# Kernel tuning notes

Measured on AMD Instinct MI355X. Metric: run time of the kernel, lower is better.

The kernel has to match this reference:

```python
import jax, jax.numpy as jnp
import numpy as np

D_MODEL = 256
D_STATE = 64
D_CONV = 4
EXPAND = 2
HEADDIM = 64
D_INNER = EXPAND * D_MODEL            # 512
NHEADS = D_INNER // HEADDIM           # 8
D_XBC = D_INNER + 2 * D_STATE         # 640 (x, B, C; ngroups=1)
D_IN_PROJ = 2 * D_INNER + 2 * D_STATE + NHEADS  # 1160


def setup_inputs() -> dict:
    key = jax.random.key(0)
    ks = jax.random.split(key, 8)
    x = jax.random.normal(ks[0], (64, 5000, 12), jnp.float32)
    W_in = jax.random.normal(ks[1], (D_MODEL, D_IN_PROJ), jnp.float32) * 0.02
    conv_w = jax.random.normal(ks[2], (D_XBC, D_CONV), jnp.float32) * 0.1
    conv_b = jnp.zeros((D_XBC,), jnp.float32)
    A_log = jnp.log(jax.random.uniform(ks[3], (NHEADS,), jnp.float32, 1.0, 16.0))
    dt_bias = jax.random.normal(ks[4], (NHEADS,), jnp.float32) * 0.1
    D = jnp.ones((NHEADS,), jnp.float32)
    norm_w = jnp.ones((D_INNER,), jnp.float32)
    W_out = jax.random.normal(ks[5], (D_INNER, D_MODEL), jnp.float32) * 0.02
    return {"x": x, "W_in": W_in, "conv_w": conv_w, "conv_b": conv_b,
            "A_log": A_log, "dt_bias": dt_bias, "D": D,
            "norm_w": norm_w, "W_out": W_out}


def _mamba2(u, W_in, conv_w, conv_b, A_log, dt_bias, D, norm_w, W_out):
    b, l, _ = u.shape
    zxbcdt = u @ W_in                                   # (b,l,1160)
    z = zxbcdt[..., :D_INNER]                           # (b,l,512)
    xBC = zxbcdt[..., D_INNER:D_INNER + D_XBC]          # (b,l,640)
    dt = zxbcdt[..., D_INNER + D_XBC:]                  # (b,l,8)
    # causal depthwise conv1d (kernel 4) + SiLU
    xp = jnp.pad(xBC, ((0, 0), (D_CONV - 1, 0), (0, 0)))
    xBC = sum(xp[:, k:k + l, :] * conv_w[:, k] for k in range(D_CONV)) + conv_b
    xBC = jax.nn.silu(xBC)
    xs = xBC[..., :D_INNER].reshape(b, l, NHEADS, HEADDIM)
    Bm = xBC[..., D_INNER:D_INNER + D_STATE]            # (b,l,64)
    Cm = xBC[..., D_INNER + D_STATE:]                   # (b,l,64)
    dt = jax.nn.softplus(dt + dt_bias)                  # (b,l,h)
    A = -jnp.exp(A_log)                                 # (h,)

    def step(h, inp):
        x_t, dt_t, B_t, C_t = inp                       # (b,h,p),(b,h),(b,n),(b,n)
        decay = jnp.exp(dt_t * A)                       # (b,h)
        h = h * decay[..., None, None] + (dt_t[..., None] * x_t)[..., None] * B_t[:, None, None, :]
        y = jnp.einsum('bhpn,bn->bhp', h, C_t)
        return h, y

    h0 = jnp.zeros((b, NHEADS, HEADDIM, D_STATE), u.dtype)
    _, ys = jax.lax.scan(step, h0, (xs.transpose(1, 0, 2, 3), dt.transpose(1, 0, 2),
                                    Bm.transpose(1, 0, 2), Cm.transpose(1, 0, 2)))
    y = ys.transpose(1, 0, 2, 3) + D[None, None, :, None] * xs   # D skip, per head
    y = y.reshape(b, l, D_INNER)
    # RMSNormGated: gate then rmsnorm
    y = y * jax.nn.silu(z)
    y = y * jax.lax.rsqrt(jnp.mean(y * y, axis=-1, keepdims=True) + 1e-5) * norm_w
    return y @ W_out                                    # (b,l,256)


def reference(x, W_in, conv_w, conv_b, A_log, dt_bias, D, norm_w, W_out):
    b = x.shape[0]
    u = x.reshape(b, 250, 240)                          # 'b (t p1) f -> b t (p1 f)'
    u = jnp.pad(u, ((0, 0), (0, 0), (0, D_MODEL - 240)))
    y = _mamba2(u, W_in, conv_w, conv_b, A_log, dt_bias, D, norm_w, W_out)
    y = jax.nn.selu(y)                                  # AlphaDropout is identity at eval
    y = y[..., :240]
    return y.reshape(b, 5000, 12)
```

## Files before the change

### kernel.cpp

```cpp
#include <hip/hip_runtime.h>
#include <cstdint>
#include <cstddef>

#define D_MODEL 256
#define D_STATE 64
#define HEADDIM 64
#define D_INNER 512
#define NHEADS 8
#define D_XBC 640
#define NPROJ 1160
#define ZXW 1152
#define BATCH 64
#define SEQ 250
#define ROWS (BATCH * SEQ)
#define KIN 240
#define KPAD 256
#define NPAD 1216
#define TPAD 256

typedef __bf16 bf16x8 __attribute__((ext_vector_type(8)));
typedef float f32x4 __attribute__((ext_vector_type(4)));

__device__ __forceinline__ float readlane_f(float v, int lane) {
    return __uint_as_float(__builtin_amdgcn_readlane(__float_as_uint(v), lane));
}
__device__ __forceinline__ float silu_f(float x) { return x * (1.f / (1.f + __expf(-x))); }
__device__ __forceinline__ unsigned short bf16_rne(float f) {
    unsigned int u = __float_as_uint(f);
    u += 0x7fff + ((u >> 16) & 1);
    return (unsigned short)(u >> 16);
}
__device__ __forceinline__ float bf2f(unsigned short u) {
    return __uint_as_float(((unsigned int)u) << 16);
}
__device__ __forceinline__ unsigned int pack2(float a, float b) {
    return (unsigned int)bf16_rne(a) | ((unsigned int)bf16_rne(b) << 16);
}

__global__ __launch_bounds__(256) void cast_w_kernel(const float* __restrict__ Win,
                                                     unsigned short* __restrict__ bt_bf) {
    int idx = blockIdx.x * 256 + threadIdx.x;
    int n = idx >> 8, k = idx & 255;
    float v = (n < NPROJ && k < KIN) ? Win[k * NPROJ + n] : 0.f;
    bt_bf[idx] = bf16_rne(v);
}

#define SB 272
__global__ __launch_bounds__(256) void gemm1_mfma(const float* __restrict__ X,
                                                  const unsigned short* __restrict__ Bt,
                                                  unsigned short* __restrict__ Czx,
                                                  float* __restrict__ dtraw) {
    __shared__ unsigned short S[64 * SB];
    const int tid = threadIdx.x;
    const int lane = tid & 63, w = tid >> 6;
    const int q = lane >> 4, l15 = lane & 15;
    const int rowBase = blockIdx.x * 64;

    {
        const int r = tid >> 2, seg = tid & 3;
        const float* xr = X + (size_t)(rowBase + r) * KIN;
#pragma unroll
        for (int i = 0; i < 15; i++) {
            int c4 = seg * 15 + i;
            float4 v = *(const float4*)&xr[c4 * 4];
            unsigned short t4[4];
            t4[0] = bf16_rne(v.x); t4[1] = bf16_rne(v.y);
            t4[2] = bf16_rne(v.z); t4[3] = bf16_rne(v.w);
            *(uint2*)&S[r * SB + c4 * 4] = *(uint2*)t4;
        }
        if (seg < 2) {
            uint4 z = {0, 0, 0, 0};
            *(uint4*)&S[r * SB + 240 + seg * 8] = z;
        }
    }
    __syncthreads();
    bf16x8 afr[8];
#pragma unroll
    for (int kk = 0; kk < 8; kk++)
        afr[kk] = *(const bf16x8*)&S[(w * 16 + l15) * SB + kk * 32 + q * 8];
    __syncthreads();

    for (int j = 0; j < 19; j++) {
        {
            const int r = tid >> 2, seg = tid & 3;
            const unsigned short* br = Bt + (size_t)(j * 64 + r) * KPAD;
#pragma unroll
            for (int i = 0; i < 8; i++) {
                int c = seg * 8 + i * 32;
                int cs = (c ^ ((r & 3) << 3));
                *(uint4*)&S[r * SB + cs] = *(const uint4*)&br[c];
            }
        }
        __syncthreads();
        f32x4 acc[4] = {};
#pragma unroll
        for (int kk = 0; kk < 8; kk++) {
#pragma unroll
            for (int nt = 0; nt < 4; nt++) {
                int row = nt * 16 + l15;
                int c = kk * 32 + q * 8;
                int cs = (c ^ ((row & 3) << 3));
                bf16x8 bfr = *(const bf16x8*)&S[row * SB + cs];
                acc[nt] = __builtin_amdgcn_mfma_f32_16x16x32_bf16(afr[kk], bfr,
                                                                  acc[nt], 0, 0, 0);
            }
        }
        __syncthreads();

        if (j < 18) {
#pragma unroll
            for (int nt = 0; nt < 4; nt++) {
                int gcol = j * 64 + nt * 16 + l15;
#pragma unroll
                for (int reg = 0; reg < 4; reg++) {
                    int grow = rowBase + w * 16 + q * 4 + reg;
                    unsigned int u = bf16_rne(acc[nt][reg]);
                    unsigned int partner = (unsigned int)__shfl_xor((int)u, 1, 64);
                    if ((l15 & 1) == 0)
                        *(unsigned int*)&Czx[(size_t)grow * ZXW + gcol] =
                            u | (partner << 16);
                }
            }
        } else {
            if (l15 < 8) {
#pragma unroll
                for (int reg = 0; reg < 4; reg++) {
                    int grow = rowBase + w * 16 + q * 4 + reg;
                    dtraw[(size_t)grow * NHEADS + l15] = acc[0][reg];
                }
            }
        }
    }
}

#define CT_IN_STR 68
#define CT_TR_STR 70
__global__ __launch_bounds__(256) void conv_kernel(const unsigned short* __restrict__ zxbc,
                                                   const float* __restrict__ dtraw,
                                                   const float* __restrict__ conv_w,
                                                   const float* __restrict__ conv_b,
                                                   const float* __restrict__ dt_bias,
                                                   unsigned short* __restrict__ xc_bf,
                                                   unsigned short* __restrict__ xcT_bf,
                                                   float* __restrict__ dtp) {
    const int b = blockIdx.x;
    const int t0 = blockIdx.z * 64;
    if (blockIdx.y == 10) {
        for (int it = threadIdx.x; it < 512; it += 256) {
            int h = it & 7;
            int t = t0 + (it >> 3);
            if (t < SEQ) {
                float v = dtraw[(size_t)(b * SEQ + t) * NHEADS + h] + dt_bias[h];
                dtp[(size_t)(b * SEQ + t) * NHEADS + h] =
                    (v > 20.f) ? v : __logf(1.f + __expf(v));
            }
        }
        return;
    }
    __shared__ float In[67 * CT_IN_STR];
    __shared__ unsigned short OutT[64 * CT_TR_STR];
    const int cg = blockIdx.y;
    const int tid = threadIdx.x;
    const int lane = tid & 63;
    const int w = tid >> 6;
    const int ch = cg * 64 + lane;

    for (int r = w; r < 67; r += 4) {
        int t = t0 - 3 + r;
        float v = (t >= 0 && t < SEQ)
                      ? bf2f(zxbc[(size_t)(b * SEQ + t) * ZXW + D_INNER + ch])
                      : 0.f;
        In[r * CT_IN_STR + lane] = v;
    }
    __syncthreads();
    const float w0 = conv_w[ch * 4 + 0], w1 = conv_w[ch * 4 + 1];
    const float w2 = conv_w[ch * 4 + 2], w3 = conv_w[ch * 4 + 3];
    const float bias = conv_b[ch];
    unsigned short vals[16];
#pragma unroll
    for (int i = 0; i < 16; i++) {
        int tt = w * 16 + i;
        float acc = fmaf(w3, In[(tt + 3) * CT_IN_STR + lane],
                    fmaf(w2, In[(tt + 2) * CT_IN_STR + lane],
                    fmaf(w1, In[(tt + 1) * CT_IN_STR + lane],
                    fmaf(w0, In[tt * CT_IN_STR + lane], bias))));
        float sv = silu_f(acc);
        unsigned short bv = (t0 + tt < SEQ) ? bf16_rne(sv) : (unsigned short)0;
        vals[i] = bv;
        OutT[lane * CT_TR_STR + tt] = bv;
    }
#pragma unroll
    for (int i = 0; i < 16; i++) {
        int tt = w * 16 + i;
        if (t0 + tt < SEQ)
            xc_bf[(size_t)(b * SEQ + t0 + tt) * D_XBC + ch] = vals[i];
    }
    __syncthreads();
    unsigned short* dstbase = xcT_bf + ((size_t)b * D_XBC + cg * 64) * TPAD + t0;
#pragma unroll
    for (int i = 0; i < 16; i++) {
        int c2 = w * 16 + i;
        dstbase[(size_t)c2 * TPAD + lane] = OutT[c2 * CT_TR_STR + lane];
    }
}

#define LSTR 72
__global__ __launch_bounds__(256) void scan_intra(const unsigned short* __restrict__ xc_bf,
                                                  const unsigned short* __restrict__ xcT_bf,
                                                  const float* __restrict__ dtp,
                                                  const float* __restrict__ A_log,
                                                  const float* __restrict__ Dvec,
                                                  unsigned short* __restrict__ yout_bf,
                                                  unsigned short* __restrict__ st_g) {
    __shared__ unsigned short C_l[64 * LSTR];
    __shared__ unsigned short BP_l[64 * LSTR];
    __shared__ unsigned short XT_l[64 * LSTR];
    __shared__ float cs_s[64], dts_s[64], fws_s[64];

    const int blk = blockIdx.x;
    const int bh = blk >> 2, c = blk & 3;
    const int b = bh >> 3, h = bh & 7;
    const int tid = threadIdx.x;
    const int lane = tid & 63, w = tid >> 6;
    const int q = lane >> 4, l15 = lane & 15;
    const int t0 = c * 64;
    const float A = -__expf(A_log[h]);
    const float Dh = Dvec[h];

    const int r = tid >> 2, c0 = (tid & 3) * 16;

    {
        if (t0 + r < SEQ) {
            const unsigned short* rowp = xc_bf + (size_t)(b * SEQ + t0 + r) * D_XBC;
            *(uint4*)&C_l[r * LSTR + c0] = *(const uint4*)&rowp[D_INNER + D_STATE + c0];
            *(uint4*)&C_l[r * LSTR + c0 + 8] =
                *(const uint4*)&rowp[D_INNER + D_STATE + c0 + 8];
            *(uint4*)&BP_l[r * LSTR + c0] = *(const uint4*)&rowp[D_INNER + c0];
            *(uint4*)&BP_l[r * LSTR + c0 + 8] = *(const uint4*)&rowp[D_INNER + c0 + 8];
        } else {
            uint4 z = {0, 0, 0, 0};
            *(uint4*)&C_l[r * LSTR + c0] = z;
            *(uint4*)&C_l[r * LSTR + c0 + 8] = z;
            *(uint4*)&BP_l[r * LSTR + c0] = z;
            *(uint4*)&BP_l[r * LSTR + c0 + 8] = z;
        }
        const unsigned short* xrow =
            xcT_bf + ((size_t)b * D_XBC + h * HEADDIM + r) * TPAD + t0;
        *(uint4*)&XT_l[r * LSTR + c0] = *(const uint4*)&xrow[c0];
        *(uint4*)&XT_l[r * LSTR + c0 + 8] = *(const uint4*)&xrow[c0 + 8];
    }
    uint4 braw0, braw1;
    {
        const unsigned short* brow =
            xcT_bf + ((size_t)b * D_XBC + D_INNER + r) * TPAD + t0 + c0;
        braw0 = *(const uint4*)&brow[0];
        braw1 = *(const uint4*)&brow[8];
    }
    if (w == 0) {
        int t = lane;
        float dtv = (t0 + t < SEQ) ? dtp[(size_t)(b * SEQ + t0 + t) * NHEADS + h] : 0.f;
        float csv = dtv * A;
#pragma unroll
        for (int o = 1; o < 64; o <<= 1) {
            float u = __shfl_up(csv, o, 64);
            if (lane >= o) csv += u;
        }
        float tot = readlane_f(csv, 63);
        cs_s[t] = csv;
        dts_s[t] = dtv;
        fws_s[t] = dtv * __expf(tot - csv);
    }
    __syncthreads();

    f32x4 g[4] = {};
#pragma unroll
    for (int k0 = 0; k0 < 64; k0 += 32) {
        bf16x8 ca = *(const bf16x8*)&C_l[(w * 16 + l15) * LSTR + k0 + q * 8];
#pragma unroll
        for (int nt = 0; nt < 4; nt++) {
            bf16x8 bb = *(const bf16x8*)&BP_l[(nt * 16 + l15) * LSTR + k0 + q * 8];
            g[nt] = __builtin_amdgcn_mfma_f32_16x16x32_bf16(ca, bb, g[nt], 0, 0, 0);
        }
    }
    __syncthreads();

    {
        unsigned short tmp[16];
        const unsigned short* rp = (const unsigned short*)&braw0;
#pragma unroll
        for (int j = 0; j < 8; j++) tmp[j] = bf16_rne(bf2f(rp[j]) * fws_s[c0 + j]);
        rp = (const unsigned short*)&braw1;
#pragma unroll
        for (int j = 0; j < 8; j++) tmp[8 + j] = bf16_rne(bf2f(rp[j]) * fws_s[c0 + 8 + j]);
        *(uint4*)&C_l[r * LSTR + c0] = *(uint4*)&tmp[0];
        *(uint4*)&C_l[r * LSTR + c0 + 8] = *(uint4*)&tmp[8];
    }
#pragma unroll
    for (int nt = 0; nt < 4; nt++) {
#pragma unroll
        for (int rr = 0; rr < 4; rr++) {
            int t = w * 16 + q * 4 + rr;
            int s = nt * 16 + l15;
            float pv = 0.f;
            if (s <= t) {
                pv = g[nt][rr] * __expf(cs_s[t] - cs_s[s]) * dts_s[s];
                if (s == t) pv += Dh;
            }
            unsigned int u = bf16_rne(pv);
            unsigned int partner = (unsigned int)__shfl_xor((int)u, 1, 64);
            if ((l15 & 1) == 0)
                *(unsigned int*)&BP_l[t * LSTR + nt * 16 + l15] = u | (partner << 16);
        }
    }
    __syncthreads();

    f32x4 y[4] = {};
#pragma unroll
    for (int k0 = 0; k0 < 64; k0 += 32) {
        bf16x8 pa = *(const bf16x8*)&BP_l[(w * 16 + l15) * LSTR + k0 + q * 8];
#pragma unroll
        for (int nt = 0; nt < 4; nt++) {
            bf16x8 xb = *(const bf16x8*)&XT_l[(nt * 16 + l15) * LSTR + k0 + q * 8];
            y[nt] = __builtin_amdgcn_mfma_f32_16x16x32_bf16(pa, xb, y[nt], 0, 0, 0);
        }
    }
    if (c < 3) {
        f32x4 st[4] = {};
#pragma unroll
        for (int k0 = 0; k0 < 64; k0 += 32) {
            bf16x8 xa = *(const bf16x8*)&XT_l[(w * 16 + l15) * LSTR + k0 + q * 8];
#pragma unroll
            for (int nt = 0; nt < 4; nt++) {
                bf16x8 bwb = *(const bf16x8*)&C_l[(nt * 16 + l15) * LSTR + k0 + q * 8];
                st[nt] = __builtin_amdgcn_mfma_f32_16x16x32_bf16(xa, bwb, st[nt], 0, 0, 0);
            }
        }
        unsigned short* stc = st_g + ((size_t)(bh * 3 + c)) * 4096;
#pragma unroll
        for (int nt = 0; nt < 4; nt++)
#pragma unroll
            for (int rr = 0; rr < 4; rr++) {
                unsigned int u = bf16_rne(st[nt][rr]);
                unsigned int partner = (unsigned int)__shfl_xor((int)u, 1, 64);
                if ((l15 & 1) == 0)
                    *(unsigned int*)&stc[(w * 16 + q * 4 + rr) * 64 + nt * 16 + l15] =
                        u | (partner << 16);
            }
    }
#pragma unroll
    for (int nt = 0; nt < 4; nt++)
#pragma unroll
        for (int rr = 0; rr < 4; rr++) {
            int t = w * 16 + q * 4 + rr;
            if (t0 + t < SEQ) {
                int p = nt * 16 + l15;
                unsigned int u = bf16_rne(y[nt][rr]);
                unsigned int partner = (unsigned int)__shfl_xor((int)u, 1, 64);
                if ((l15 & 1) == 0)
                    *(unsigned int*)&yout_bf[(size_t)(b * SEQ + t0 + t) * D_INNER +
                                             h * HEADDIM + p] = u | (partner << 16);
            }
        }
}

__global__ __launch_bounds__(256) void scan_inter(const unsigned short* __restrict__ xc_bf,
                                                  const float* __restrict__ dtp,
                                                  const float* __restrict__ A_log,
                                                  unsigned short* __restrict__ yout_bf,
                                                  const unsigned short* __restrict__ st_g) {
    __shared__ unsigned short C_l[64 * LSTR];
    __shared__ unsigned short h_l[64 * LSTR];
    __shared__ float cs_s[64];
    __shared__ float csum[4];

    const int blk = blockIdx.x;
    const int bh = blk / 3, c = (blk - bh * 3) + 1;
    const int b = bh >> 3, h = bh & 7;
    const int tid = threadIdx.x;
    const int lane = tid & 63, w = tid >> 6;
    const int q = lane >> 4, l15 = lane & 15;
    const int t0 = c * 64;
    const float A = -__expf(A_log[h]);

    {
        int t = lane;
        int gt = w * 64 + t;
        float dtv = (gt < SEQ) ? dtp[(size_t)(b * SEQ + gt) * NHEADS + h] : 0.f;
        float csv = dtv * A;
#pragma unroll
        for (int o = 1; o < 64; o <<= 1) {
            float u = __shfl_up(csv, o, 64);
            if (lane >= o) csv += u;
        }
        if (w == c) cs_s[t] = csv;
        if (lane == 63) csum[w] = csv;
    }
    {
        int r = tid >> 2, c0 = (tid & 3) * 16;
        if (t0 + r < SEQ) {
            const unsigned short* rowp = xc_bf + (size_t)(b * SEQ + t0 + r) * D_XBC;
            *(uint4*)&C_l[r * LSTR + c0] = *(const uint4*)&rowp[D_INNER + D_STATE + c0];
            *(uint4*)&C_l[r * LSTR + c0 + 8] =
                *(const uint4*)&rowp[D_INNER + D_STATE + c0 + 8];
        } else {
            uint4 z = {0, 0, 0, 0};
            *(uint4*)&C_l[r * LSTR + c0] = z;
            *(uint4*)&C_l[r * LSTR + c0 + 8] = z;
        }
    }
    __syncthreads();

    {
        float wgt[3];
        for (int cp = 0; cp < c; cp++) {
            float s = 0.f;
            for (int j = cp + 1; j < c; j++) s += csum[j];
            wgt[cp] = __expf(s);
        }
        const unsigned short* stb = st_g + (size_t)bh * 3 * 4096;
        for (int i = tid; i < 4096; i += 256) {
            float acc = 0.f;
            for (int cp = 0; cp < c; cp++) acc += wgt[cp] * bf2f(stb[cp * 4096 + i]);
            h_l[(i >> 6) * LSTR + (i & 63)] = bf16_rne(acc);
        }
    }
    __syncthreads();

    f32x4 in[4] = {};
#pragma unroll
    for (int k0 = 0; k0 < 64; k0 += 32) {
        bf16x8 ca = *(const bf16x8*)&C_l[(w * 16 + l15) * LSTR + k0 + q * 8];
#pragma unroll
        for (int nt = 0; nt < 4; nt++) {
            bf16x8 hb = *(const bf16x8*)&h_l[(nt * 16 + l15) * LSTR + k0 + q * 8];
            in[nt] = __builtin_amdgcn_mfma_f32_16x16x32_bf16(ca, hb, in[nt], 0, 0, 0);
        }
    }
#pragma unroll
    for (int nt = 0; nt < 4; nt++)
#pragma unroll
        for (int r = 0; r < 4; r++) {
            int t = w * 16 + q * 4 + r;
            if (t0 + t < SEQ) {
                int p = nt * 16 + l15;
                size_t ai = (size_t)(b * SEQ + t0 + t) * D_INNER + h * HEADDIM + p;
                float alpha = __expf(cs_s[t]);
                float nv = bf2f(yout_bf[ai]) + alpha * in[nt][r];
                unsigned int u = bf16_rne(nv);
                unsigned int partner = (unsigned int)__shfl_xor((int)u, 1, 64);
                if ((l15 & 1) == 0)
                    *(unsigned int*)&yout_bf[ai] = u | (partner << 16);
            }
        }
}

__global__ __launch_bounds__(256) void wcast_kernel(const float* __restrict__ Wout,
                                                    unsigned short* __restrict__ wt_bf) {
    int idx = blockIdx.x * 256 + threadIdx.x;
    int n = idx & 255, k = idx >> 8;
    wt_bf[n * D_INNER + k] = bf16_rne(Wout[k * D_MODEL + n]);
}

__global__ __launch_bounds__(256) void gate_kernel(const unsigned short* __restrict__ yout_bf,
                                                   const unsigned short* __restrict__ zxbc,
                                                   const float* __restrict__ norm_w,
                                                   unsigned short* __restrict__ g_bf) {
    const int wid = threadIdx.x >> 6, lane = threadIdx.x & 63;
    const int row = blockIdx.x * 4 + wid;
    const unsigned short* yr = yout_bf + (size_t)row * D_INNER;
    const unsigned short* zr = zxbc + (size_t)row * ZXW;
    const int c0 = lane * 8;
    uint4 yp = *(const uint4*)&yr[c0];
    uint4 zp = *(const uint4*)&zr[c0];
    const unsigned short* ys = (const unsigned short*)&yp;
    const unsigned short* zs = (const unsigned short*)&zp;
    float g[8];
#pragma unroll
    for (int i = 0; i < 8; i++) g[i] = bf2f(ys[i]) * silu_f(bf2f(zs[i]));
    float s = 0.f;
#pragma unroll
    for (int i = 0; i < 8; i++) s = fmaf(g[i], g[i], s);
#pragma unroll
    for (int o = 32; o; o >>= 1) s += __shfl_xor(s, o, 64);
    float rms = rsqrtf(s * (1.f / 512.f) + 1e-5f);
    float4 w0 = *(const float4*)&norm_w[c0], w1 = *(const float4*)&norm_w[c0 + 4];
    uint4 pk;
    pk.x = pack2(g[0] * rms * w0.x, g[1] * rms * w0.y);
    pk.y = pack2(g[2] * rms * w0.z, g[3] * rms * w0.w);
    pk.z = pack2(g[4] * rms * w1.x, g[5] * rms * w1.y);
    pk.w = pack2(g[6] * rms * w1.z, g[7] * rms * w1.w);
    *(uint4*)&g_bf[(size_t)row * D_INNER + c0] = pk;
}

#define SA 40
__global__ __launch_bounds__(256) void gemm2_mfma(const unsigned short* __restrict__ A,
                                                  const unsigned short* __restrict__ Bt,
                                                  float* __restrict__ out) {
    __shared__ unsigned short As[128 * SA];
    __shared__ unsigned short Bs[64 * SA];
    const int tid = threadIdx.x;
    const int lane = tid & 63, wave = tid >> 6;
    const int wm = wave >> 1, wn = wave & 1;
    const int q = lane >> 4, l15 = lane & 15;
    const int rowBase = blockIdx.y * 128, colBase = blockIdx.x * 64;
    f32x4 acc[4][2] = {};

    const int sr = tid >> 2;
    const int sc = (tid & 3) * 8;

    for (int k0 = 0; k0 < D_INNER; k0 += 32) {
        *(float4*)&As[sr * SA + sc] =
            *(const float4*)&A[(size_t)(rowBase + sr) * D_INNER + k0 + sc];
        *(float4*)&As[(sr + 64) * SA + sc] =
            *(const float4*)&A[(size_t)(rowBase + sr + 64) * D_INNER + k0 + sc];
        *(float4*)&Bs[sr * SA + sc] =
            *(const float4*)&Bt[(size_t)(colBase + sr) * D_INNER + k0 + sc];
        __syncthreads();

        bf16x8 bfr[2];
#pragma unroll
        for (int nt = 0; nt < 2; nt++)
            bfr[nt] = *(const bf16x8*)&Bs[(wn * 32 + nt * 16 + l15) * SA + q * 8];
#pragma unroll
        for (int mt = 0; mt < 4; mt++) {
            bf16x8 afr = *(const bf16x8*)&As[(wm * 64 + mt * 16 + l15) * SA + q * 8];
#pragma unroll
            for (int nt = 0; nt < 2; nt++)
                acc[mt][nt] = __builtin_amdgcn_mfma_f32_16x16x32_bf16(afr, bfr[nt],
                                                                      acc[mt][nt], 0, 0, 0);
        }
        __syncthreads();
    }
    const float SC = 1.0507009873554805f, AL = 1.6732632423543772f;
#pragma unroll
    for (int mt = 0; mt < 4; mt++) {
        int grow = rowBase + wm * 64 + mt * 16 + q * 4;
#pragma unroll
        for (int nt = 0; nt < 2; nt++) {
            int gcol = colBase + wn * 32 + nt * 16 + l15;
            if (gcol < 240) {
#pragma unroll
                for (int reg = 0; reg < 4; reg++) {
                    float v = acc[mt][nt][reg];
                    v = (v > 0.f) ? SC * v : SC * AL * (__expf(v) - 1.f);
                    out[(size_t)(grow + reg) * 240 + gcol] = v;
                }
            }
        }
    }
}

extern "C" void kernel_launch(void* const* d_in, const int* in_sizes, int n_in,
                              void* d_out, int out_size, void* d_ws, size_t ws_size,
                              hipStream_t stream) {
    const float* x = (const float*)d_in[0];
    const float* W_in = (const float*)d_in[1];
    const float* conv_w = (const float*)d_in[2];
    const float* conv_b = (const float*)d_in[3];
    const float* A_log = (const float*)d_in[4];
    const float* dt_bias = (const float*)d_in[5];
    const float* Dv = (const float*)d_in[6];
    const float* norm_w = (const float*)d_in[7];
    const float* W_out = (const float*)d_in[8];
    float* out = (float*)d_out;

    unsigned short* us = (unsigned short*)d_ws;
    unsigned short* zxbc_bf = us;
    unsigned short* xc_bf = zxbc_bf + (size_t)ROWS * ZXW;
    unsigned short* xcT_bf = xc_bf + (size_t)ROWS * D_XBC;
    unsigned short* yout_bf = xcT_bf + (size_t)BATCH * D_XBC * TPAD;
    unsigned short* st_g = yout_bf + (size_t)ROWS * D_INNER;
    unsigned short* bt_bf = st_g + (size_t)512 * 3 * 4096;
    unsigned short* wt_bf = bt_bf + (size_t)NPAD * KPAD;
    unsigned short* g_bf = wt_bf + (size_t)D_MODEL * D_INNER;
    float* dtraw = (float*)(g_bf + (size_t)ROWS * D_INNER);
    float* dtp = dtraw + (size_t)ROWS * NHEADS;

    cast_w_kernel<<<dim3(NPAD * KPAD / 256), 256, 0, stream>>>(W_in, bt_bf);

    gemm1_mfma<<<dim3(ROWS / 64), 256, 0, stream>>>(x, bt_bf, zxbc_bf, dtraw);

    conv_kernel<<<dim3(BATCH, 11, 4), 256, 0, stream>>>(zxbc_bf, dtraw, conv_w, conv_b,
                                                        dt_bias, xc_bf, xcT_bf, dtp);

    scan_intra<<<dim3(BATCH * NHEADS * 4), 256, 0, stream>>>(xc_bf, xcT_bf, dtp, A_log, Dv,
                                                             yout_bf, st_g);

    scan_inter<<<dim3(BATCH * NHEADS * 3), 256, 0, stream>>>(xc_bf, dtp, A_log,
                                                             yout_bf, st_g);

    wcast_kernel<<<dim3(D_INNER * D_MODEL / 256), 256, 0, stream>>>(W_out, wt_bf);

    gate_kernel<<<dim3(ROWS / 4), 256, 0, stream>>>(yout_bf, zxbc_bf, norm_w, g_bf);

    gemm2_mfma<<<dim3(D_MODEL / 64, ROWS / 128), 256, 0, stream>>>(g_bf, wt_bf, out);
}
```

Measured before the change: 223.2 us.

## Split gemm1 column tiles across two blocks, prefetch B into registers, transpose MFMA output

```diff
diff --git a/kernel.cpp b/kernel.cpp
--- a/kernel.cpp
+++ b/kernel.cpp
@@ -54,10 +54,13 @@
     const int tid = threadIdx.x;
     const int lane = tid & 63, w = tid >> 6;
     const int q = lane >> 4, l15 = lane & 15;
-    const int rowBase = blockIdx.x * 64;
-
-    {
-        const int r = tid >> 2, seg = tid & 3;
+    const int rowBase = blockIdx.y * 64;
+    const int jBeg = blockIdx.x * 10;
+    const int jEnd = (jBeg + 10 < 19) ? jBeg + 10 : 19;
+
+    const int r = tid >> 2, seg = tid & 3;
+
+    {
         const float* xr = X + (size_t)(rowBase + r) * KIN;
 #pragma unroll
         for (int i = 0; i < 15; i++) {
@@ -78,20 +81,31 @@
 #pragma unroll
     for (int kk = 0; kk < 8; kk++)
         afr[kk] = *(const bf16x8*)&S[(w * 16 + l15) * SB + kk * 32 + q * 8];
-    __syncthreads();
-
-    for (int j = 0; j < 19; j++) {
-        {
-            const int r = tid >> 2, seg = tid & 3;
-            const unsigned short* br = Bt + (size_t)(j * 64 + r) * KPAD;
-#pragma unroll
-            for (int i = 0; i < 8; i++) {
-                int c = seg * 8 + i * 32;
-                int cs = (c ^ ((r & 3) << 3));
-                *(uint4*)&S[r * SB + cs] = *(const uint4*)&br[c];
-            }
-        }
+
+    uint4 breg[8];
+    {
+        const unsigned short* br = Bt + (size_t)(jBeg * 64 + r) * KPAD;
+#pragma unroll
+        for (int i = 0; i < 8; i++)
+            breg[i] = *(const uint4*)&br[seg * 8 + i * 32];
+    }
+
+    for (int j = jBeg; j < jEnd; j++) {
         __syncthreads();
+#pragma unroll
+        for (int i = 0; i < 8; i++) {
+            int c = seg * 8 + i * 32;
+            int cs = c ^ ((r & 3) << 3);
+            *(uint4*)&S[r * SB + cs] = breg[i];
+        }
+        if (j + 1 < jEnd) {
+            const unsigned short* br = Bt + (size_t)((j + 1) * 64 + r) * KPAD;
+#pragma unroll
+            for (int i = 0; i < 8; i++)
+                breg[i] = *(const uint4*)&br[seg * 8 + i * 32];
+        }
+        __syncthreads();
+
         f32x4 acc[4] = {};
 #pragma unroll
         for (int kk = 0; kk < 8; kk++) {
@@ -99,36 +113,26 @@
             for (int nt = 0; nt < 4; nt++) {
                 int row = nt * 16 + l15;
                 int c = kk * 32 + q * 8;
-                int cs = (c ^ ((row & 3) << 3));
+                int cs = c ^ ((row & 3) << 3);
                 bf16x8 bfr = *(const bf16x8*)&S[row * SB + cs];
-                acc[nt] = __builtin_amdgcn_mfma_f32_16x16x32_bf16(afr[kk], bfr,
+                acc[nt] = __builtin_amdgcn_mfma_f32_16x16x32_bf16(bfr, afr[kk],
                                                                   acc[nt], 0, 0, 0);
             }
         }
-        __syncthreads();
-
+        const int grow = rowBase + w * 16 + l15;
         if (j < 18) {
 #pragma unroll
             for (int nt = 0; nt < 4; nt++) {
-                int gcol = j * 64 + nt * 16 + l15;
-#pragma unroll
-                for (int reg = 0; reg < 4; reg++) {
-                    int grow = rowBase + w * 16 + q * 4 + reg;
-                    unsigned int u = bf16_rne(acc[nt][reg]);
-                    unsigned int partner = (unsigned int)__shfl_xor((int)u, 1, 64);
-                    if ((l15 & 1) == 0)
-                        *(unsigned int*)&Czx[(size_t)grow * ZXW + gcol] =
-                            u | (partner << 16);
-                }
-            }
-        } else {
-            if (l15 < 8) {
-#pragma unroll
-                for (int reg = 0; reg < 4; reg++) {
-                    int grow = rowBase + w * 16 + q * 4 + reg;
-                    dtraw[(size_t)grow * NHEADS + l15] = acc[0][reg];
-                }
-            }
+                int gcol = j * 64 + nt * 16 + q * 4;
+                uint2 pk;
+                pk.x = pack2(acc[nt][0], acc[nt][1]);
+                pk.y = pack2(acc[nt][2], acc[nt][3]);
+                *(uint2*)&Czx[(size_t)grow * ZXW + gcol] = pk;
+            }
+        } else if (q < 2) {
+#pragma unroll
+            for (int reg = 0; reg < 4; reg++)
+                dtraw[(size_t)grow * NHEADS + q * 4 + reg] = acc[0][reg];
         }
     }
 }
@@ -578,7 +582,7 @@
 
     cast_w_kernel<<<dim3(NPAD * KPAD / 256), 256, 0, stream>>>(W_in, bt_bf);
 
-    gemm1_mfma<<<dim3(ROWS / 64), 256, 0, stream>>>(x, bt_bf, zxbc_bf, dtraw);
+    gemm1_mfma<<<dim3(2, ROWS / 64), 256, 0, stream>>>(x, bt_bf, zxbc_bf, dtraw);
 
     conv_kernel<<<dim3(BATCH, 11, 4), 256, 0, stream>>>(zxbc_bf, dtraw, conv_w, conv_b,
                                                         dt_bias, xc_bf, xcT_bf, dtp);
```

Result: slower. 245.1 us (+9.8%).
